# Kernel optimization log

Hardware: AMD Instinct MI355X
Metric: run time of the kernel (lower is better)

The kernel has to match this reference:

```python
import jax, jax.numpy as jnp
import numpy as np

N = 1024          # num_nodes
IN_DIM = 16
HID = 32
OUT_DIM = 256
NUM_BLOCKS = 3
E = 8192
F = N * HID       # flattened_dim = 32768


def gcn_conv(x, W, b, row, col):
    """PyG-style GCNConv: symmetric normalization with self-loops.
    row/col already include self-loops. Messages flow row -> col."""
    h = x @ W                                   # [N, out]
    deg = jax.ops.segment_sum(jnp.ones_like(col, dtype=h.dtype), col, num_segments=N)
    dinv = jnp.where(deg > 0, jax.lax.rsqrt(jnp.maximum(deg, 1e-12)), 0.0)
    norm = dinv[row] * dinv[col]                # [E+N]
    msg = h[row] * norm[:, None]                # gather + scale
    out = jax.ops.segment_sum(msg, col, num_segments=N)
    return out + b


def setup_inputs() -> dict:
    key = jax.random.key(0)
    ks = jax.random.split(key, 12)
    x = jax.random.normal(ks[0], (N, IN_DIM), dtype=jnp.float32)
    edge_index = jax.random.randint(ks[1], (2, E), 0, N, dtype=jnp.int32)
    s = 0.05
    W_in = jax.random.normal(ks[2], (IN_DIM, HID), dtype=jnp.float32) * s
    b_in = jnp.zeros((HID,), dtype=jnp.float32)
    Wb = jax.random.normal(ks[3], (NUM_BLOCKS, 2, HID, HID), dtype=jnp.float32) * s
    bb = jnp.zeros((NUM_BLOCKS, 2, HID), dtype=jnp.float32)
    W1 = jax.random.normal(ks[4], (F, F // 4), dtype=jnp.float32) * 0.005
    b1 = jnp.zeros((F // 4,), dtype=jnp.float32)
    W2 = jax.random.normal(ks[5], (F // 4, F // 8), dtype=jnp.float32) * 0.01
    b2 = jnp.zeros((F // 8,), dtype=jnp.float32)
    W3 = jax.random.normal(ks[6], (F // 8, OUT_DIM), dtype=jnp.float32) * 0.02
    b3 = jnp.zeros((OUT_DIM,), dtype=jnp.float32)
    return {"x": x, "edge_index": edge_index, "W_in": W_in, "b_in": b_in,
            "Wb": Wb, "bb": bb, "W1": W1, "b1": b1, "W2": W2, "b2": b2,
            "W3": W3, "b3": b3}


def reference(x, edge_index, W_in, b_in, Wb, bb, W1, b1, W2, b2, W3, b3):
    # add self-loops once (shared by all conv layers)
    loops = jnp.arange(N, dtype=edge_index.dtype)
    row = jnp.concatenate([edge_index[0], loops])
    col = jnp.concatenate([edge_index[1], loops])

    h = jax.nn.relu(gcn_conv(x, W_in, b_in, row, col))
    for blk in range(NUM_BLOCKS):
        identity = h
        o = jax.nn.relu(gcn_conv(h, Wb[blk, 0], bb[blk, 0], row, col))
        o = gcn_conv(o, Wb[blk, 1], bb[blk, 1], row, col)
        h = jax.nn.relu(o + identity)

    v = h.reshape(-1)                      # [F]
    v = jax.nn.relu(v @ W1 + b1)
    v = jax.nn.relu(v @ W2 + b2)
    v = v @ W3 + b3
    return jax.nn.softmax(v, axis=-1)
```

## Files before the change

### kernel.cpp

```cpp
#include <hip/hip_runtime.h>

#define NN      1024
#define IN_DIM  16
#define HID     32
#define OUT_DIM 256
#define NE      8192
#define FDIM    (NN*HID)
#define F4      (FDIM/4)
#define F8      (FDIM/8)
#define MAXNB   48

typedef float f4 __attribute__((ext_vector_type(4)));

__global__ void __launch_bounds__(1024) csr_k(
    const int* __restrict__ row, const int* __restrict__ col,
    float* __restrict__ deg_g, int* __restrict__ off_g,
    int* __restrict__ nrow, float* __restrict__ nw)
{
    __shared__ float degs[NN];
    __shared__ int   curs[NN];
    __shared__ int   scan[NN];
    const int t = threadIdx.x;
    degs[t] = 1.f;
    __syncthreads();
    for (int e = t; e < NE; e += 1024) atomicAdd(&degs[col[e]], 1.f);
    __syncthreads();
    int c = (int)degs[t] - 1;
    scan[t] = c;
    __syncthreads();
    for (int d = 1; d < 1024; d <<= 1) {
        int v = (t >= d) ? scan[t - d] : 0;
        __syncthreads();
        scan[t] += v;
        __syncthreads();
    }
    int excl = scan[t] - c;
    curs[t] = excl;
    off_g[t] = excl;
    deg_g[t] = degs[t];
    __syncthreads();
    for (int e = t; e < NE; e += 1024) {
        int r = row[e], cc = col[e];
        int slot = atomicAdd(&curs[cc], 1);
        nrow[slot] = r;
        nw[slot] = rsqrtf(degs[r] * degs[cc]);
    }
}

template<int K, int RELU_IN, int EPI>
__global__ void __launch_bounds__(256) conv_k(
    const float* __restrict__ IN, const float* __restrict__ RES,
    const float* __restrict__ W, const float* __restrict__ bias,
    const float* __restrict__ deg, const int* __restrict__ off,
    const int* __restrict__ nrow, const float* __restrict__ nw,
    float* __restrict__ OUT)
{
    const int n = blockIdx.x;
    const int tid = threadIdx.x;
    const int s = tid >> 5, f = tid & 31;
    __shared__ float rows[MAXNB][K + 4];
    __shared__ float part[8][33];
    const int base = off[n];
    const int cnt = (int)deg[n] - 1;
    const int tot = cnt + 1;
    const int stg = tot < MAXNB ? tot : MAXNB;
    const int vecs = K / 4;
    for (int idx = tid; idx < stg * vecs; idx += 256) {
        int j = idx / vecs, q = idx - j * vecs;
        int r = (j == 0) ? n : nrow[base + j - 1];
        float4 val = *reinterpret_cast<const float4*>(IN + r * K + q * 4);
        if (RELU_IN) {
            val.x = fmaxf(val.x, 0.f); val.y = fmaxf(val.y, 0.f);
            val.z = fmaxf(val.z, 0.f); val.w = fmaxf(val.w, 0.f);
        }
        rows[j][q * 4 + 0] = val.x; rows[j][q * 4 + 1] = val.y;
        rows[j][q * 4 + 2] = val.z; rows[j][q * 4 + 3] = val.w;
    }
    __syncthreads();
    float acc = 0.f;
    for (int j = s; j < tot; j += 8) {
        float w = (j == 0) ? (1.0f / deg[n]) : nw[base + j - 1];
        float hw = 0.f;
        if (j < MAXNB) {
            #pragma unroll
            for (int k = 0; k < K; ++k)
                hw = fmaf(rows[j][k], W[k * HID + f], hw);
        } else {
            const float* inr = IN + nrow[base + j - 1] * K;
            #pragma unroll
            for (int k = 0; k < K; ++k) {
                float t = inr[k];
                if (RELU_IN) t = fmaxf(t, 0.f);
                hw = fmaf(t, W[k * HID + f], hw);
            }
        }
        acc = fmaf(w, hw, acc);
    }
    part[s][f] = acc;
    __syncthreads();
    if (s == 0) {
        float tot_v = bias[f];
        #pragma unroll
        for (int q = 0; q < 8; ++q) tot_v += part[q][f];
        int i = n * HID + f;
        if (EPI == 0)      OUT[i] = tot_v;
        else if (EPI == 1) OUT[i] = tot_v + fmaxf(RES[i], 0.f);
        else               OUT[i] = fmaxf(tot_v + fmaxf(RES[i], 0.f), 0.f);
    }
}

template<int R>
__global__ void __launch_bounds__(256) gemv_part_k(
    const float* __restrict__ v, const float* __restrict__ W,
    float* __restrict__ part, int cols)
{
    const int col0 = blockIdx.x * 1024 + threadIdx.x * 4;
    const int row0 = blockIdx.y * R;
    const f4* vq = reinterpret_cast<const f4*>(v + row0);
    const float* Wp = W + (size_t)row0 * cols + col0;
    f4 acc = {0.f, 0.f, 0.f, 0.f};
    #pragma unroll 4
    for (int rq = 0; rq < R / 4; ++rq) {
        f4 s4 = vq[rq];
        const float* Wr = Wp + (size_t)(rq * 4) * cols;
        if (s4.x != 0.f) { f4 w = __builtin_nontemporal_load((const f4*)(Wr));            acc += s4.x * w; }
        if (s4.y != 0.f) { f4 w = __builtin_nontemporal_load((const f4*)(Wr + cols));     acc += s4.y * w; }
        if (s4.z != 0.f) { f4 w = __builtin_nontemporal_load((const f4*)(Wr + 2 * cols)); acc += s4.z * w; }
        if (s4.w != 0.f) { f4 w = __builtin_nontemporal_load((const f4*)(Wr + 3 * cols)); acc += s4.w * w; }
    }
    *reinterpret_cast<f4*>(part + (size_t)blockIdx.y * cols + col0) = acc;
}

template<int SPLITS>
__global__ void __launch_bounds__(256) reduce_bias_relu_k(
    const float* __restrict__ part, const float* __restrict__ b,
    float* __restrict__ y, int cols)
{
    __shared__ float red[256];
    const int t = threadIdx.x;
    const int jj = t & 63;
    const int g = t >> 6;
    const int j = blockIdx.x * 64 + jj;
    float acc = 0.f;
    #pragma unroll 4
    for (int s = g; s < SPLITS; s += 4)
        acc += part[(size_t)s * cols + j];
    red[t] = acc;
    __syncthreads();
    if (g == 0) {
        float tot = b[j] + red[jj] + red[64 + jj] + red[128 + jj] + red[192 + jj];
        y[j] = fmaxf(tot, 0.f);
    }
}

template<int R>
__global__ void __launch_bounds__(256) gemv3_k(
    const float* __restrict__ v, const float* __restrict__ W,
    float* __restrict__ part)
{
    const int t = threadIdx.x;
    const int row0 = blockIdx.x * R;
    float acc = 0.f;
    #pragma unroll 8
    for (int r = 0; r < R; ++r) {
        float s = v[row0 + r];
        if (s != 0.f)
            acc = fmaf(s, __builtin_nontemporal_load(&W[(size_t)(row0 + r) * OUT_DIM + t]), acc);
    }
    part[blockIdx.x * OUT_DIM + t] = acc;
}

template<int SPLITS>
__global__ void __launch_bounds__(256) softmax_k(
    const float* __restrict__ part3, const float* __restrict__ b3,
    float* __restrict__ out)
{
    __shared__ float red[256];
    const int t = threadIdx.x;
    float acc = b3[t];
    #pragma unroll 8
    for (int s = 0; s < SPLITS; ++s) acc += part3[s * OUT_DIM + t];
    red[t] = acc;
    __syncthreads();
    for (int k = 128; k > 0; k >>= 1) {
        if (t < k) red[t] = fmaxf(red[t], red[t + k]);
        __syncthreads();
    }
    float m = red[0];
    __syncthreads();
    float e = expf(acc - m);
    red[t] = e;
    __syncthreads();
    for (int k = 128; k > 0; k >>= 1) {
        if (t < k) red[t] += red[t + k];
        __syncthreads();
    }
    out[t] = e / red[0];
}

extern "C" void kernel_launch(void* const* d_in, const int* in_sizes, int n_in,
                              void* d_out, int out_size, void* d_ws, size_t ws_size,
                              hipStream_t stream) {
    const float* x    = (const float*)d_in[0];
    const int*   ei   = (const int*)  d_in[1];
    const float* W_in = (const float*)d_in[2];
    const float* b_in = (const float*)d_in[3];
    const float* Wb   = (const float*)d_in[4];
    const float* bb   = (const float*)d_in[5];
    const float* W1   = (const float*)d_in[6];
    const float* b1   = (const float*)d_in[7];
    const float* W2   = (const float*)d_in[8];
    const float* b2   = (const float*)d_in[9];
    const float* W3   = (const float*)d_in[10];
    const float* b3   = (const float*)d_in[11];
    float* out = (float*)d_out;

    const int* row = ei;
    const int* col = ei + NE;

    float* ws    = (float*)d_ws;
    float* deg   = ws;
    int*   off   = (int*)(deg + NN);
    int*   nrow  = off + NN;
    float* nw    = (float*)(nrow + NE);
    float* H1    = nw + NE;
    float* H2    = H1 + FDIM;
    float* H3    = H2 + FDIM;
    float* T     = H3 + FDIM;
    float* v     = T + FDIM;
    float* part1 = v + FDIM;
    float* y1    = part1 + 256 * F4;
    float* part2 = y1 + F4;
    float* y2    = part2 + 256 * F8;
    float* part3 = y2 + F8;

    csr_k<<<1, 1024, 0, stream>>>(row, col, deg, off, nrow, nw);

    conv_k<IN_DIM, 0, 0><<<NN, 256, 0, stream>>>(x,  nullptr, W_in, b_in, deg, off, nrow, nw, H1);
    conv_k<HID, 1, 0><<<NN, 256, 0, stream>>>(H1, nullptr, Wb + 0*HID*HID, bb + 0*HID, deg, off, nrow, nw, T);
    conv_k<HID, 1, 1><<<NN, 256, 0, stream>>>(T,  H1,      Wb + 1*HID*HID, bb + 1*HID, deg, off, nrow, nw, H2);
    conv_k<HID, 1, 0><<<NN, 256, 0, stream>>>(H2, nullptr, Wb + 2*HID*HID, bb + 2*HID, deg, off, nrow, nw, T);
    conv_k<HID, 1, 1><<<NN, 256, 0, stream>>>(T,  H2,      Wb + 3*HID*HID, bb + 3*HID, deg, off, nrow, nw, H3);
    conv_k<HID, 1, 0><<<NN, 256, 0, stream>>>(H3, nullptr, Wb + 4*HID*HID, bb + 4*HID, deg, off, nrow, nw, T);
    conv_k<HID, 1, 2><<<NN, 256, 0, stream>>>(T,  H3,      Wb + 5*HID*HID, bb + 5*HID, deg, off, nrow, nw, v);

    {
        dim3 g(F4 / 1024, FDIM / 128);
        gemv_part_k<128><<<g, 256, 0, stream>>>(v, W1, part1, F4);
        reduce_bias_relu_k<256><<<F4 / 64, 256, 0, stream>>>(part1, b1, y1, F4);
    }
    {
        dim3 g(F8 / 1024, F4 / 32);
        gemv_part_k<32><<<g, 256, 0, stream>>>(y1, W2, part2, F8);
        reduce_bias_relu_k<256><<<F8 / 64, 256, 0, stream>>>(part2, b2, y2, F8);
    }
    {
        gemv3_k<32><<<F8 / 32, 256, 0, stream>>>(y2, W3, part3);
        softmax_k<128><<<1, 256, 0, stream>>>(part3, b3, out);
    }
}
```

Baseline: 235.3 us.

## Compact nonzero activations before MLP GEMVs to balance sparse row work

Adds a single-block prefix-scan kernel that compacts the nonzero entries of each MLP input vector into (index, value) pairs. The GEMV kernels then split the compacted list evenly across blocks instead of fixed row ranges with per-row zero branches. This targets load imbalance and divergent branching from ReLU sparsity, so work scales with the nonzero count. The cost is three extra single-block serial launches and an added dependent load of the nonzero count.

```diff
diff --git a/kernel.cpp b/kernel.cpp
--- a/kernel.cpp
+++ b/kernel.cpp
@@ -109,26 +109,60 @@
     }
 }
 
-template<int R>
-__global__ void __launch_bounds__(256) gemv_part_k(
-    const float* __restrict__ v, const float* __restrict__ W,
-    float* __restrict__ part, int cols)
+template<int NELEM>
+__global__ void __launch_bounds__(1024) compact_k(
+    const float* __restrict__ y, int2* __restrict__ nz, int* __restrict__ nnz_out)
+{
+    constexpr int PER = NELEM / 1024;
+    const int t = threadIdx.x;
+    const int base = t * PER;
+    float vals[PER];
+    int cnt = 0;
+    #pragma unroll
+    for (int i = 0; i < PER; ++i) {
+        vals[i] = y[base + i];
+        cnt += (vals[i] != 0.f) ? 1 : 0;
+    }
+    __shared__ int sc[1024];
+    sc[t] = cnt;
+    __syncthreads();
+    for (int d = 1; d < 1024; d <<= 1) {
+        int v = (t >= d) ? sc[t - d] : 0;
+        __syncthreads();
+        sc[t] += v;
+        __syncthreads();
+    }
+    int off = sc[t] - cnt;
+    #pragma unroll
+    for (int i = 0; i < PER; ++i) {
+        if (vals[i] != 0.f) {
+            int2 p; p.x = base + i; p.y = __float_as_int(vals[i]);
+            nz[off++] = p;
+        }
+    }
+    if (t == 1023) *nnz_out = sc[1023];
+}
+
+template<int SHIFT>
+__global__ void __launch_bounds__(256) gemv_nz_k(
+    const int2* __restrict__ nz, const int* __restrict__ nnz_p,
+    const float* __restrict__ W, float* __restrict__ part, int cols)
 {
     const int col0 = blockIdx.x * 1024 + threadIdx.x * 4;
-    const int row0 = blockIdx.y * R;
-    const f4* vq = reinterpret_cast<const f4*>(v + row0);
-    const float* Wp = W + (size_t)row0 * cols + col0;
+    const int nnz = *nnz_p;
+    const int s = blockIdx.y;
+    const int lo = (int)(((long long)s * nnz) >> SHIFT);
+    const int hi = (int)(((long long)(s + 1) * nnz) >> SHIFT);
     f4 acc = {0.f, 0.f, 0.f, 0.f};
     #pragma unroll 4
-    for (int rq = 0; rq < R / 4; ++rq) {
-        f4 s4 = vq[rq];
-        const float* Wr = Wp + (size_t)(rq * 4) * cols;
-        if (s4.x != 0.f) { f4 w = __builtin_nontemporal_load((const f4*)(Wr));            acc += s4.x * w; }
-        if (s4.y != 0.f) { f4 w = __builtin_nontemporal_load((const f4*)(Wr + cols));     acc += s4.y * w; }
-        if (s4.z != 0.f) { f4 w = __builtin_nontemporal_load((const f4*)(Wr + 2 * cols)); acc += s4.z * w; }
-        if (s4.w != 0.f) { f4 w = __builtin_nontemporal_load((const f4*)(Wr + 3 * cols)); acc += s4.w * w; }
-    }
-    *reinterpret_cast<f4*>(part + (size_t)blockIdx.y * cols + col0) = acc;
+    for (int i = lo; i < hi; ++i) {
+        int2 p = nz[i];
+        float val = __int_as_float(p.y);
+        f4 w = __builtin_nontemporal_load(
+            reinterpret_cast<const f4*>(W + (size_t)p.x * cols + col0));
+        acc += val * w;
+    }
+    *reinterpret_cast<f4*>(part + (size_t)s * cols + col0) = acc;
 }
 
 template<int SPLITS>
@@ -153,21 +187,24 @@
     }
 }
 
-template<int R>
-__global__ void __launch_bounds__(256) gemv3_k(
-    const float* __restrict__ v, const float* __restrict__ W,
-    float* __restrict__ part)
-{
-    const int t = threadIdx.x;
-    const int row0 = blockIdx.x * R;
+template<int SHIFT>
+__global__ void __launch_bounds__(256) gemv3_nz_k(
+    const int2* __restrict__ nz, const int* __restrict__ nnz_p,
+    const float* __restrict__ W, float* __restrict__ part)
+{
+    const int t = threadIdx.x;
+    const int nnz = *nnz_p;
+    const int s = blockIdx.x;
+    const int lo = (int)(((long long)s * nnz) >> SHIFT);
+    const int hi = (int)(((long long)(s + 1) * nnz) >> SHIFT);
     float acc = 0.f;
-    #pragma unroll 8
-    for (int r = 0; r < R; ++r) {
-        float s = v[row0 + r];
-        if (s != 0.f)
-            acc = fmaf(s, __builtin_nontemporal_load(&W[(size_t)(row0 + r) * OUT_DIM + t]), acc);
-    }
-    part[blockIdx.x * OUT_DIM + t] = acc;
+    #pragma unroll 4
+    for (int i = lo; i < hi; ++i) {
+        int2 p = nz[i];
+        acc = fmaf(__int_as_float(p.y),
+                   __builtin_nontemporal_load(&W[(size_t)p.x * OUT_DIM + t]), acc);
+    }
+    part[s * OUT_DIM + t] = acc;
 }
 
 template<int SPLITS>
@@ -233,6 +270,10 @@
     float* part2 = y1 + F4;
     float* y2    = part2 + 256 * F8;
     float* part3 = y2 + F8;
+    int2*  nz1   = (int2*)(part3 + 128 * OUT_DIM);
+    int2*  nz2   = nz1 + FDIM;
+    int2*  nz3   = nz2 + F4;
+    int*   nnz   = (int*)(nz3 + F8);
 
     csr_k<<<1, 1024, 0, stream>>>(row, col, deg, off, nrow, nw);
 
@@ -244,18 +285,21 @@
     conv_k<HID, 1, 0><<<NN, 256, 0, stream>>>(H3, nullptr, Wb + 4*HID*HID, bb + 4*HID, deg, off, nrow, nw, T);
     conv_k<HID, 1, 2><<<NN, 256, 0, stream>>>(T,  H3,      Wb + 5*HID*HID, bb + 5*HID, deg, off, nrow, nw, v);
 
+    compact_k<FDIM><<<1, 1024, 0, stream>>>(v, nz1, nnz + 0);
     {
-        dim3 g(F4 / 1024, FDIM / 128);
-        gemv_part_k<128><<<g, 256, 0, stream>>>(v, W1, part1, F4);
+        dim3 g(F4 / 1024, 256);
+        gemv_nz_k<8><<<g, 256, 0, stream>>>(nz1, nnz + 0, W1, part1, F4);
         reduce_bias_relu_k<256><<<F4 / 64, 256, 0, stream>>>(part1, b1, y1, F4);
     }
+    compact_k<F4><<<1, 1024, 0, stream>>>(y1, nz2, nnz + 1);
     {
-        dim3 g(F8 / 1024, F4 / 32);
-        gemv_part_k<32><<<g, 256, 0, stream>>>(y1, W2, part2, F8);
+        dim3 g(F8 / 1024, 256);
+        gemv_nz_k<8><<<g, 256, 0, stream>>>(nz2, nnz + 1, W2, part2, F8);
         reduce_bias_relu_k<256><<<F8 / 64, 256, 0, stream>>>(part2, b2, y2, F8);
     }
+    compact_k<F8><<<1, 1024, 0, stream>>>(y2, nz3, nnz + 2);
     {
-        gemv3_k<32><<<F8 / 32, 256, 0, stream>>>(y2, W3, part3);
+        gemv3_nz_k<7><<<128, 256, 0, stream>>>(nz3, nnz + 2, W3, part3);
         softmax_k<128><<<1, 256, 0, stream>>>(part3, b3, out);
     }
 }
```

Measured after the change: 276.5 us. 17.5% more time.
